# Kernel optimization log

Hardware: AMD Instinct MI355X
Metric: run time of the kernel (lower is better)

## Reference

```python
import jax, jax.numpy as jnp
import numpy as np

B, C, H, W = 16, 256, 96, 96
K = 3
K2 = K * K


def setup_inputs() -> dict:
    key = jax.random.key(0)
    ks = jax.random.split(key, 8)
    s = 1.0 / np.sqrt(C)  # fan-in style scale for 1x1 convs
    sk = 1.0 / np.sqrt(K2)
    return {
        "x": jax.random.normal(ks[0], (B, C, H, W), jnp.float32),
        "w_xproj": jax.random.normal(ks[1], (C, C), jnp.float32) * s,
        "b_xproj": jnp.zeros((C,), jnp.float32),
        "w_proj": jax.random.normal(ks[2], (C, C), jnp.float32) * s,
        "b_proj": jnp.zeros((C,), jnp.float32),
        "w_kp": jax.random.normal(ks[3], (C, C), jnp.float32) * s,
        "b_kp": jnp.zeros((C,), jnp.float32),
        "w_kg": jax.random.normal(ks[4], (K2, K2), jnp.float32) * sk,
        "b_kg": jnp.zeros((K2,), jnp.float32),
        "diff_ctrl": jnp.zeros((1, 1, 1, C), jnp.float32),
    }


def reference(x, w_xproj, b_xproj, w_proj, b_proj, w_kp, b_kp, w_kg, b_kg, diff_ctrl):
    b, c, h, w = x.shape
    # --- kernel synthesis ---
    # 1x1 conv (kernel_proj)
    kp = jnp.einsum('bchw,oc->bohw', x, w_kp) + b_kp[None, :, None, None]
    # AdaptiveAvgPool1d over flattened spatial dim -> 9 bins (H*W divisible by 9)
    pooled = kp.reshape(b, c, K2, (h * w) // K2).mean(axis=-1)  # [B, C, 9]
    pooled = jax.nn.gelu(pooled)
    # per-channel Linear(9 -> 9): y = W @ v + b
    ker = jnp.einsum('bck,jk->bcj', pooled, w_kg) + b_kg  # [B, C, 9]
    # rearrange 'c (k1 k2) -> k1 k2 1 c' (batched)
    ker = ker.reshape(b, c, K, K).transpose(0, 2, 3, 1)[:, :, :, None, :]  # [B, K, K, 1, C]
    # lateral inhibition: subtract learned fraction of per-channel kernel mean
    factor = jax.nn.sigmoid(diff_ctrl)  # [1, 1, 1, C]
    ker = ker - factor * ker.mean(axis=(1, 2, 3), keepdims=True)
    # --- main path ---
    xp = jnp.einsum('bchw,oc->bohw', x, w_xproj) + b_xproj[None, :, None, None]
    pad = K // 2

    def dwconv(xi, ki):  # xi [C,H,W], ki [K,K,1,C]
        return jax.lax.conv_general_dilated(
            xi[None], ki, window_strides=(1, 1),
            padding=((pad, pad), (pad, pad)),
            dimension_numbers=('NCHW', 'HWIO', 'NCHW'),
            feature_group_count=c)[0]

    y = jax.vmap(dwconv)(xp, ker)  # per-sample dynamic depthwise conv
    out = jnp.einsum('bchw,oc->bohw', y, w_proj) + b_proj[None, :, None, None]
    return out
```

## Files before the change

kernel.cpp:

```cpp
#include <hip/hip_runtime.h>

#define CCH 256
#define HWP 9216
#define IMGDIM 96

typedef __attribute__((ext_vector_type(8))) short s16x8;
typedef __attribute__((ext_vector_type(4))) float f32x4;

__device__ __forceinline__ unsigned short f2bf(float f){
  unsigned u = __float_as_uint(f);
  u += 0x7fffu + ((u >> 16) & 1u);
  return (unsigned short)(u >> 16);
}
__device__ __forceinline__ float bf2f(unsigned short h){
  return __uint_as_float(((unsigned)h) << 16);
}

__global__ void k0_convert(const float* __restrict__ wx, const float* __restrict__ wp,
                           unsigned short* __restrict__ wxb, unsigned short* __restrict__ wpb){
  int i = blockIdx.x * 256 + threadIdx.x;
  wxb[i] = f2bf(wx[i]);
  wpb[i] = f2bf(wp[i]);
}

__device__ __forceinline__ void gemm_core(const unsigned short* __restrict__ wbf,
                                          const unsigned short* lds_x,
                                          f32x4 acc[4][4], int lane, int obase){
  const int g = lane >> 4, r = lane & 15;
  #pragma unroll
  for (int k0 = 0; k0 < 256; k0 += 32){
    s16x8 afr[4], bfr[4];
    #pragma unroll
    for (int nf = 0; nf < 4; ++nf){
      int p = nf*16 + r;
      unsigned off = (unsigned)(p*512 + (k0 + g*8)*2) ^ ((unsigned)(p & 7) << 4);
      bfr[nf] = *(const s16x8*)((const char*)lds_x + off);
    }
    #pragma unroll
    for (int mf = 0; mf < 4; ++mf){
      afr[mf] = *(const s16x8*)(wbf + (size_t)(obase + mf*16 + r)*CCH + k0 + g*8);
    }
    #pragma unroll
    for (int mf = 0; mf < 4; ++mf){
      #pragma unroll
      for (int nf = 0; nf < 4; ++nf){
        acc[mf][nf] = __builtin_amdgcn_mfma_f32_16x16x32_bf16(afr[mf], bfr[nf], acc[mf][nf], 0, 0, 0);
      }
    }
  }
}

__global__ __launch_bounds__(256) void k1_xproj(const float* __restrict__ x,
    const unsigned short* __restrict__ wxb, const float* __restrict__ bx,
    unsigned short* __restrict__ xp, float* __restrict__ xpart){
  const int tile = blockIdx.x, b = blockIdx.y;
  const int p0 = tile * 64;
  const int t = threadIdx.x;
  const int lane = t & 63, wave = t >> 6;
  __shared__ __align__(16) unsigned short xlds[64*256];

  const float* xb = x + (size_t)b * CCH * HWP;
  const int binj = p0 >> 10;
  const int blk  = (p0 >> 6) & 15;
  const int pg = t & 15;
  const int cgl = t >> 4;

  #pragma unroll
  for (int i = 0; i < 4; ++i){
    const int c0 = (i*16 + cgl) * 4;
    const int pl = pg * 4;
    float v[4][4];
    #pragma unroll
    for (int ci = 0; ci < 4; ++ci){
      float4 q = *(const float4*)(xb + (size_t)(c0 + ci)*HWP + p0 + pl);
      v[ci][0]=q.x; v[ci][1]=q.y; v[ci][2]=q.z; v[ci][3]=q.w;
    }
    #pragma unroll
    for (int pj = 0; pj < 4; ++pj){
      const int p = pl + pj;
      unsigned off = (unsigned)(p*512 + c0*2) ^ ((unsigned)(p & 7) << 4);
      ushort4 pk;
      pk.x = f2bf(v[0][pj]); pk.y = f2bf(v[1][pj]);
      pk.z = f2bf(v[2][pj]); pk.w = f2bf(v[3][pj]);
      *(ushort4*)((char*)xlds + off) = pk;
    }
    #pragma unroll
    for (int ci = 0; ci < 4; ++ci){
      float s = v[ci][0] + v[ci][1] + v[ci][2] + v[ci][3];
      s += __shfl_xor(s, 1); s += __shfl_xor(s, 2);
      s += __shfl_xor(s, 4); s += __shfl_xor(s, 8);
      if ((lane & 15) == 0){
        xpart[(((size_t)b*9 + binj)*16 + blk)*CCH + (c0 + ci)] = s;
      }
    }
  }
  __syncthreads();

  f32x4 acc[4][4];
  f32x4 zz = {0.f,0.f,0.f,0.f};
  #pragma unroll
  for (int i2=0;i2<4;++i2){
    #pragma unroll
    for (int j2=0;j2<4;++j2) acc[i2][j2] = zz;
  }
  gemm_core(wxb, xlds, acc, lane, wave*64);

  const int g = lane >> 4, r = lane & 15;
  #pragma unroll
  for (int mf = 0; mf < 4; ++mf){
    const int o = wave*64 + mf*16 + 4*g;
    float b0 = bx[o], b1 = bx[o+1], b2 = bx[o+2], b3 = bx[o+3];
    #pragma unroll
    for (int nf = 0; nf < 4; ++nf){
      const int p = p0 + nf*16 + r;
      ushort4 pk;
      pk.x = f2bf(acc[mf][nf][0] + b0);
      pk.y = f2bf(acc[mf][nf][1] + b1);
      pk.z = f2bf(acc[mf][nf][2] + b2);
      pk.w = f2bf(acc[mf][nf][3] + b3);
      *(ushort4*)(xp + ((size_t)b*HWP + p)*CCH + o) = pk;
    }
  }
}

__global__ __launch_bounds__(256) void k2a_pooled(const float* __restrict__ xpart,
    const float* __restrict__ wkp, const float* __restrict__ bkp,
    float* __restrict__ pooledg){
  const int j = blockIdx.x, b = blockIdx.y, t = threadIdx.x;
  __shared__ float xbar[256];
  __shared__ float wch[256][65];
  const float* xp0 = xpart + (((size_t)b*9 + j)*16)*CCH;
  float s = 0.f;
  #pragma unroll
  for (int blk = 0; blk < 16; ++blk) s += xp0[blk*CCH + t];
  xbar[t] = s * (1.0f/1024.0f);
  float acc = bkp[t];
  for (int ch = 0; ch < 4; ++ch){
    __syncthreads();
    for (int u = t; u < 256*64; u += 256){
      wch[u >> 6][u & 63] = wkp[(size_t)(u >> 6)*CCH + ch*64 + (u & 63)];
    }
    __syncthreads();
    #pragma unroll
    for (int c = 0; c < 64; ++c) acc += wch[t][c] * xbar[ch*64 + c];
  }
  float x3 = acc*acc*acc;
  float tg = tanhf(0.7978845608028654f*(acc + 0.044715f*x3));
  pooledg[((size_t)b*9 + j)*CCH + t] = 0.5f*acc*(1.0f + tg);
}

__global__ void k2b_ker(const float* __restrict__ pooledg, const float* __restrict__ wkg,
                        const float* __restrict__ bkg, const float* __restrict__ dctrl,
                        float* __restrict__ kerg){
  const int b = blockIdx.x, c = threadIdx.x;
  float pl[9];
  #pragma unroll
  for (int k = 0; k < 9; ++k) pl[k] = pooledg[((size_t)b*9 + k)*CCH + c];
  float kv[9]; float m = 0.f;
  #pragma unroll
  for (int jp = 0; jp < 9; ++jp){
    float s2 = bkg[jp];
    #pragma unroll
    for (int k = 0; k < 9; ++k) s2 += pl[k] * wkg[jp*9 + k];
    kv[jp] = s2; m += s2;
  }
  m *= (1.0f/9.0f);
  float f = 1.0f / (1.0f + expf(-dctrl[c]));
  #pragma unroll
  for (int jp = 0; jp < 9; ++jp) kerg[((size_t)b*9 + jp)*CCH + c] = kv[jp] - f*m;
}

__global__ __launch_bounds__(256) void k3_conv(const unsigned short* __restrict__ xp,
    const unsigned short* __restrict__ wpb, const float* __restrict__ bp,
    const float* __restrict__ kerg, float* __restrict__ out){
  const int tile = blockIdx.x, b = blockIdx.y;
  const int th0 = (tile / 12) * 8, tw0 = (tile % 12) * 8;
  const int t = threadIdx.x, lane = t & 63, wave = t >> 6;
  __shared__ __align__(16) unsigned short halo[100*128];
  __shared__ __align__(16) unsigned short ylds[64*256];
  __shared__ __align__(16) float kl[9][256];

  for (int u = t; u < 9*256; u += 256)
    kl[u >> 8][u & 255] = kerg[((size_t)b*9 + (u >> 8))*CCH + (u & 255)];

  const unsigned short* xpb = xp + (size_t)b * HWP * CCH;
  const int p = t & 63, dh = p >> 3, dw = p & 7;
  const int clb = (t >> 6) * 32;

  for (int chunk = 0; chunk < 2; ++chunk){
    __syncthreads();
    for (int u = t; u < 1600; u += 256){
      const int pos = u >> 4, w16 = u & 15;
      const int rr = pos / 10, cc = pos % 10;
      const int hh = th0 + rr - 1, ww = tw0 + cc - 1;
      uint4 val = {0u,0u,0u,0u};
      if (hh >= 0 && hh < IMGDIM && ww >= 0 && ww < IMGDIM)
        val = *(const uint4*)(xpb + ((size_t)(hh*IMGDIM + ww))*CCH + chunk*128 + w16*8);
      unsigned off = (unsigned)(pos*256 + w16*16) ^ ((unsigned)(pos & 7) << 4);
      *(uint4*)((char*)halo + off) = val;
    }
    __syncthreads();
    #pragma unroll
    for (int ci = 0; ci < 4; ++ci){
      const int cl = clb + ci*8;
      const int cg = chunk*128 + cl;
      float a8[8] = {0,0,0,0,0,0,0,0};
      #pragma unroll
      for (int tap = 0; tap < 9; ++tap){
        const int pos = (dh + tap/3)*10 + (dw + tap%3);
        unsigned hof = (unsigned)(pos*256 + cl*2) ^ ((unsigned)(pos & 7) << 4);
        union { uint4 q; unsigned short u16[8]; } hv;
        hv.q = *(const uint4*)((const char*)halo + hof);
        const float4* kp4 = (const float4*)&kl[tap][cg];
        float4 ka = kp4[0], kb = kp4[1];
        a8[0] += bf2f(hv.u16[0]) * ka.x;
        a8[1] += bf2f(hv.u16[1]) * ka.y;
        a8[2] += bf2f(hv.u16[2]) * ka.z;
        a8[3] += bf2f(hv.u16[3]) * ka.w;
        a8[4] += bf2f(hv.u16[4]) * kb.x;
        a8[5] += bf2f(hv.u16[5]) * kb.y;
        a8[6] += bf2f(hv.u16[6]) * kb.z;
        a8[7] += bf2f(hv.u16[7]) * kb.w;
      }
      unsigned pk[4];
      #pragma unroll
      for (int e = 0; e < 4; ++e)
        pk[e] = (unsigned)f2bf(a8[2*e]) | ((unsigned)f2bf(a8[2*e+1]) << 16);
      unsigned yoff = (unsigned)(p*512 + cg*2) ^ ((unsigned)(p & 7) << 4);
      *(uint4*)((char*)ylds + yoff) = *(uint4*)pk;
    }
  }
  __syncthreads();

  f32x4 acc[4][4];
  f32x4 zz = {0.f,0.f,0.f,0.f};
  #pragma unroll
  for (int i2=0;i2<4;++i2){
    #pragma unroll
    for (int j2=0;j2<4;++j2) acc[i2][j2] = zz;
  }
  gemm_core(wpb, ylds, acc, lane, wave*64);

  const int g = lane >> 4, r = lane & 15;
  #pragma unroll
  for (int mf = 0; mf < 4; ++mf){
    const int o = wave*64 + mf*16 + 4*g;
    float b0 = bp[o], b1 = bp[o+1], b2 = bp[o+2], b3 = bp[o+3];
    #pragma unroll
    for (int nf = 0; nf < 4; ++nf){
      const int pl2 = nf*16 + r;
      const int hh = th0 + (pl2 >> 3), ww = tw0 + (pl2 & 7);
      const size_t pix = (size_t)hh*IMGDIM + ww;
      out[((size_t)b*CCH + o + 0)*HWP + pix] = acc[mf][nf][0] + b0;
      out[((size_t)b*CCH + o + 1)*HWP + pix] = acc[mf][nf][1] + b1;
      out[((size_t)b*CCH + o + 2)*HWP + pix] = acc[mf][nf][2] + b2;
      out[((size_t)b*CCH + o + 3)*HWP + pix] = acc[mf][nf][3] + b3;
    }
  }
}

extern "C" void kernel_launch(void* const* d_in, const int* in_sizes, int n_in,
                              void* d_out, int out_size, void* d_ws, size_t ws_size,
                              hipStream_t stream){
  const float* x   = (const float*)d_in[0];
  const float* wxp = (const float*)d_in[1];
  const float* bxp = (const float*)d_in[2];
  const float* wpr = (const float*)d_in[3];
  const float* bpr = (const float*)d_in[4];
  const float* wkp = (const float*)d_in[5];
  const float* bkp = (const float*)d_in[6];
  const float* wkg = (const float*)d_in[7];
  const float* bkg = (const float*)d_in[8];
  const float* dct = (const float*)d_in[9];

  char* ws = (char*)d_ws;
  unsigned short* xp    = (unsigned short*)(ws);
  float*          xpart = (float*)(ws + 75497472);
  float*          pooled= (float*)(ws + 77856768);
  float*          kerg  = (float*)(ws + 78004224);
  unsigned short* wxb   = (unsigned short*)(ws + 78151680);
  unsigned short* wpb   = (unsigned short*)(ws + 78282752);
  float* o = (float*)d_out;

  k0_convert<<<256, 256, 0, stream>>>(wxp, wpr, wxb, wpb);
  k1_xproj<<<dim3(144,16), 256, 0, stream>>>(x, wxb, bxp, xp, xpart);
  k2a_pooled<<<dim3(9,16), 256, 0, stream>>>(xpart, wkp, bkp, pooled);
  k2b_ker<<<16, 256, 0, stream>>>(pooled, wkg, bkg, dct, kerg);
  k3_conv<<<dim3(144,16), 256, 0, stream>>>(xp, wpb, bpr, kerg, o);
}
```

Measured before the change: 278.0 us.

## Split fused depthwise+projection kernel and stage xproj stores through LDS

The fused depthwise-conv plus 1x1 projection kernel is split into two kernels: a depthwise conv that writes a bf16 intermediate buffer, then a separate GEMM projection. The split only runs when the workspace is large enough, otherwise the fused kernel is kept. The xproj epilogue now stages its output tile through a swizzled LDS buffer so global stores are full 16-byte contiguous writes. The split trades an extra round trip through global memory (about 75MB of writes and reads) for simpler kernels with less LDS per block and possibly higher occupancy.

```diff
diff --git a/kernel.cpp b/kernel.cpp
--- a/kernel.cpp
+++ b/kernel.cpp
@@ -105,20 +105,36 @@
   }
   gemm_core(wxb, xlds, acc, lane, wave*64);
 
-  const int g = lane >> 4, r = lane & 15;
-  #pragma unroll
-  for (int mf = 0; mf < 4; ++mf){
-    const int o = wave*64 + mf*16 + 4*g;
-    float b0 = bx[o], b1 = bx[o+1], b2 = bx[o+2], b3 = bx[o+3];
-    #pragma unroll
-    for (int nf = 0; nf < 4; ++nf){
-      const int p = p0 + nf*16 + r;
-      ushort4 pk;
-      pk.x = f2bf(acc[mf][nf][0] + b0);
-      pk.y = f2bf(acc[mf][nf][1] + b1);
-      pk.z = f2bf(acc[mf][nf][2] + b2);
-      pk.w = f2bf(acc[mf][nf][3] + b3);
-      *(ushort4*)(xp + ((size_t)b*HWP + p)*CCH + o) = pk;
+  __syncthreads();
+  {
+    const int g = lane >> 4, r = lane & 15;
+    #pragma unroll
+    for (int mf = 0; mf < 4; ++mf){
+      const int o = wave*64 + mf*16 + 4*g;
+      float b0 = bx[o], b1 = bx[o+1], b2 = bx[o+2], b3 = bx[o+3];
+      #pragma unroll
+      for (int nf = 0; nf < 4; ++nf){
+        const int p = nf*16 + r;
+        unsigned off = (unsigned)(p*512 + o*2) ^ ((unsigned)(p & 7) << 4);
+        ushort4 pk;
+        pk.x = f2bf(acc[mf][nf][0] + b0);
+        pk.y = f2bf(acc[mf][nf][1] + b1);
+        pk.z = f2bf(acc[mf][nf][2] + b2);
+        pk.w = f2bf(acc[mf][nf][3] + b3);
+        *(ushort4*)((char*)xlds + off) = pk;
+      }
+    }
+  }
+  __syncthreads();
+  {
+    const size_t gbase = ((size_t)b*HWP + p0)*CCH;
+    #pragma unroll
+    for (int it = 0; it < 8; ++it){
+      const unsigned u = it*256 + t;
+      const unsigned p = u >> 5;
+      const unsigned srcoff = (u*16u) ^ ((p & 7) << 4);
+      uint4 v = *(const uint4*)((const char*)xlds + srcoff);
+      *(uint4*)(xp + gbase + (size_t)u*8) = v;
     }
   }
 }
@@ -168,6 +184,112 @@
   float f = 1.0f / (1.0f + expf(-dctrl[c]));
   #pragma unroll
   for (int jp = 0; jp < 9; ++jp) kerg[((size_t)b*9 + jp)*CCH + c] = kv[jp] - f*m;
+}
+
+__global__ __launch_bounds__(256) void k3a_dw(const unsigned short* __restrict__ xp,
+    const float* __restrict__ kerg, unsigned short* __restrict__ y){
+  const int tile = blockIdx.x, b = blockIdx.y;
+  const int th0 = (tile / 12) * 8, tw0 = (tile % 12) * 8;
+  const int t = threadIdx.x;
+  __shared__ __align__(16) unsigned short halo[100*128];
+  __shared__ float kl[9][256];
+
+  for (int u = t; u < 9*256; u += 256)
+    kl[u >> 8][u & 255] = kerg[((size_t)b*9 + (u >> 8))*CCH + (u & 255)];
+
+  const unsigned short* xpb = xp + (size_t)b * HWP * CCH;
+  unsigned short* yb = y + (size_t)b * HWP * CCH;
+  const int p = t >> 2;
+  const int dh = p >> 3, dw = p & 7;
+  const int cl = (t & 3) * 8;
+  const size_t pout = (size_t)((th0 + dh)*IMGDIM + (tw0 + dw))*CCH;
+
+  for (int chunk = 0; chunk < 2; ++chunk){
+    __syncthreads();
+    for (int u = t; u < 1600; u += 256){
+      const int pos = u >> 4, w16 = u & 15;
+      const int rr = pos / 10, cc = pos % 10;
+      const int hh = th0 + rr - 1, ww = tw0 + cc - 1;
+      uint4 val = {0u,0u,0u,0u};
+      if (hh >= 0 && hh < IMGDIM && ww >= 0 && ww < IMGDIM)
+        val = *(const uint4*)(xpb + ((size_t)(hh*IMGDIM + ww))*CCH + chunk*128 + w16*8);
+      unsigned off = (unsigned)(pos*256 + w16*16) ^ ((unsigned)(pos & 7) << 4);
+      *(uint4*)((char*)halo + off) = val;
+    }
+    __syncthreads();
+    #pragma unroll
+    for (int ci = 0; ci < 4; ++ci){
+      const int c = cl + ci*32;
+      const int cg = chunk*128 + c;
+      float a8[8] = {0,0,0,0,0,0,0,0};
+      #pragma unroll
+      for (int tap = 0; tap < 9; ++tap){
+        const int pos = (dh + tap/3)*10 + (dw + tap%3);
+        unsigned hof = (unsigned)(pos*256 + c*2) ^ ((unsigned)(pos & 7) << 4);
+        union { uint4 q; unsigned short u16[8]; } hv;
+        hv.q = *(const uint4*)((const char*)halo + hof);
+        const float4* kp4 = (const float4*)&kl[tap][cg];
+        float4 ka = kp4[0], kb = kp4[1];
+        a8[0] += bf2f(hv.u16[0]) * ka.x;
+        a8[1] += bf2f(hv.u16[1]) * ka.y;
+        a8[2] += bf2f(hv.u16[2]) * ka.z;
+        a8[3] += bf2f(hv.u16[3]) * ka.w;
+        a8[4] += bf2f(hv.u16[4]) * kb.x;
+        a8[5] += bf2f(hv.u16[5]) * kb.y;
+        a8[6] += bf2f(hv.u16[6]) * kb.z;
+        a8[7] += bf2f(hv.u16[7]) * kb.w;
+      }
+      unsigned pk[4];
+      #pragma unroll
+      for (int e = 0; e < 4; ++e)
+        pk[e] = (unsigned)f2bf(a8[2*e]) | ((unsigned)f2bf(a8[2*e+1]) << 16);
+      *(uint4*)(yb + pout + cg) = *(uint4*)pk;
+    }
+  }
+}
+
+__global__ __launch_bounds__(256) void k3b_proj(const unsigned short* __restrict__ y,
+    const unsigned short* __restrict__ wpb, const float* __restrict__ bp,
+    float* __restrict__ out){
+  const int tile = blockIdx.x, b = blockIdx.y;
+  const int p0 = tile * 64;
+  const int t = threadIdx.x, lane = t & 63, wave = t >> 6;
+  __shared__ __align__(16) unsigned short ylds[64*256];
+  const unsigned short* yb = y + (size_t)b * HWP * CCH;
+
+  #pragma unroll
+  for (int it = 0; it < 8; ++it){
+    const unsigned u = it*256 + t;
+    const unsigned p = u >> 5;
+    const unsigned c16 = (u & 31) ^ (p & 7);
+    uint4 v = *(const uint4*)(yb + (size_t)(p0 + p)*CCH + c16*8);
+    *(uint4*)((char*)ylds + (size_t)u*16) = v;
+  }
+  __syncthreads();
+
+  f32x4 acc[4][4];
+  f32x4 zz = {0.f,0.f,0.f,0.f};
+  #pragma unroll
+  for (int i2=0;i2<4;++i2){
+    #pragma unroll
+    for (int j2=0;j2<4;++j2) acc[i2][j2] = zz;
+  }
+  gemm_core(wpb, ylds, acc, lane, wave*64);
+
+  const int g = lane >> 4, r = lane & 15;
+  #pragma unroll
+  for (int mf = 0; mf < 4; ++mf){
+    const int o = wave*64 + mf*16 + 4*g;
+    float b0 = bp[o], b1 = bp[o+1], b2 = bp[o+2], b3 = bp[o+3];
+    #pragma unroll
+    for (int nf = 0; nf < 4; ++nf){
+      const int pp = p0 + nf*16 + r;
+      out[((size_t)b*CCH + o + 0)*HWP + pp] = acc[mf][nf][0] + b0;
+      out[((size_t)b*CCH + o + 1)*HWP + pp] = acc[mf][nf][1] + b1;
+      out[((size_t)b*CCH + o + 2)*HWP + pp] = acc[mf][nf][2] + b2;
+      out[((size_t)b*CCH + o + 3)*HWP + pp] = acc[mf][nf][3] + b3;
+    }
+  }
 }
 
 __global__ __launch_bounds__(256) void k3_conv(const unsigned short* __restrict__ xp,
@@ -274,17 +396,24 @@
   const float* dct = (const float*)d_in[9];
 
   char* ws = (char*)d_ws;
-  unsigned short* xp    = (unsigned short*)(ws);
-  float*          xpart = (float*)(ws + 75497472);
-  float*          pooled= (float*)(ws + 77856768);
-  float*          kerg  = (float*)(ws + 78004224);
-  unsigned short* wxb   = (unsigned short*)(ws + 78151680);
-  unsigned short* wpb   = (unsigned short*)(ws + 78282752);
+  unsigned short* wxb   = (unsigned short*)(ws + 0);
+  unsigned short* wpb   = (unsigned short*)(ws + 131072);
+  float*          xpart = (float*)(ws + 262144);
+  float*          pooled= (float*)(ws + 2621440);
+  float*          kerg  = (float*)(ws + 2768896);
+  unsigned short* xp    = (unsigned short*)(ws + 2916352);
+  unsigned short* ybuf  = (unsigned short*)(ws + 78413824);
+  const size_t need_split = 153911296;
   float* o = (float*)d_out;
 
   k0_convert<<<256, 256, 0, stream>>>(wxp, wpr, wxb, wpb);
   k1_xproj<<<dim3(144,16), 256, 0, stream>>>(x, wxb, bxp, xp, xpart);
   k2a_pooled<<<dim3(9,16), 256, 0, stream>>>(xpart, wkp, bkp, pooled);
   k2b_ker<<<16, 256, 0, stream>>>(pooled, wkg, bkg, dct, kerg);
-  k3_conv<<<dim3(144,16), 256, 0, stream>>>(xp, wpb, bpr, kerg, o);
-}
+  if (ws_size >= need_split){
+    k3a_dw<<<dim3(144,16), 256, 0, stream>>>(xp, kerg, ybuf);
+    k3b_proj<<<dim3(144,16), 256, 0, stream>>>(ybuf, wpb, bpr, o);
+  } else {
+    k3_conv<<<dim3(144,16), 256, 0, stream>>>(xp, wpb, bpr, kerg, o);
+  }
+}
```

Result: faster. 238.7 us (-14.1%).

## Split depthwise conv and projection, double-buffer LDS channel chunks, stage epilogue stores

Applied to the files above, without the earlier changes.

The xproj GEMM now streams channel chunks of 64 through double-buffered LDS, loading the next chunk while computing the current one. Its output goes out through an LDS staging buffer so global stores are coalesced. The fused conv+proj kernel is split into a depthwise kernel, which writes a bf16 intermediate to global memory, and a separate pipelined projection GEMM kernel with contiguous 64-pixel tiles. The goal is to cut LDS footprint and raise occupancy, and to overlap loads with compute. The cost is an extra intermediate round-trip through HBM, roughly 75MB written and read, plus an extra launch.

```diff
diff --git a/kernel.cpp b/kernel.cpp
--- a/kernel.cpp
+++ b/kernel.cpp
@@ -23,23 +23,23 @@
   wpb[i] = f2bf(wp[i]);
 }
 
-__device__ __forceinline__ void gemm_core(const unsigned short* __restrict__ wbf,
-                                          const unsigned short* lds_x,
-                                          f32x4 acc[4][4], int lane, int obase){
+__device__ __forceinline__ void gemm_chunk(const unsigned short* __restrict__ wbf,
+                                           const unsigned short* buf,
+                                           f32x4 acc[4][4], int lane, int obase, int c0){
   const int g = lane >> 4, r = lane & 15;
   #pragma unroll
-  for (int k0 = 0; k0 < 256; k0 += 32){
+  for (int kk = 0; kk < 2; ++kk){
+    const int kc = kk*32 + g*8;
     s16x8 afr[4], bfr[4];
     #pragma unroll
     for (int nf = 0; nf < 4; ++nf){
-      int p = nf*16 + r;
-      unsigned off = (unsigned)(p*512 + (k0 + g*8)*2) ^ ((unsigned)(p & 7) << 4);
-      bfr[nf] = *(const s16x8*)((const char*)lds_x + off);
-    }
-    #pragma unroll
-    for (int mf = 0; mf < 4; ++mf){
-      afr[mf] = *(const s16x8*)(wbf + (size_t)(obase + mf*16 + r)*CCH + k0 + g*8);
-    }
+      const int p = nf*16 + r;
+      unsigned off = (unsigned)(p*128 + kc*2) ^ ((unsigned)(p & 7) << 4);
+      bfr[nf] = *(const s16x8*)((const char*)buf + off);
+    }
+    #pragma unroll
+    for (int mf = 0; mf < 4; ++mf)
+      afr[mf] = *(const s16x8*)(wbf + (size_t)(obase + mf*16 + r)*CCH + c0 + kc);
     #pragma unroll
     for (int mf = 0; mf < 4; ++mf){
       #pragma unroll
@@ -50,52 +50,48 @@
   }
 }
 
+__device__ __forceinline__ void k1_load(const float* __restrict__ xb, int p0, int c0,
+                                        int pg, int cgl, float v[4][4]){
+  #pragma unroll
+  for (int ci = 0; ci < 4; ++ci){
+    float4 q = *(const float4*)(xb + (size_t)(c0 + cgl*4 + ci)*HWP + p0 + pg*4);
+    v[ci][0]=q.x; v[ci][1]=q.y; v[ci][2]=q.z; v[ci][3]=q.w;
+  }
+}
+__device__ __forceinline__ void k1_store(unsigned short* buf, int pg, int cgl, float v[4][4],
+                                         float* __restrict__ xpart, int c0, int lane, int bbase){
+  #pragma unroll
+  for (int pj = 0; pj < 4; ++pj){
+    const int p = pg*4 + pj;
+    unsigned off = (unsigned)(p*128 + cgl*8) ^ ((unsigned)(p & 7) << 4);
+    ushort4 pk;
+    pk.x = f2bf(v[0][pj]); pk.y = f2bf(v[1][pj]);
+    pk.z = f2bf(v[2][pj]); pk.w = f2bf(v[3][pj]);
+    *(ushort4*)((char*)buf + off) = pk;
+  }
+  #pragma unroll
+  for (int ci = 0; ci < 4; ++ci){
+    float s = v[ci][0] + v[ci][1] + v[ci][2] + v[ci][3];
+    s += __shfl_xor(s, 1); s += __shfl_xor(s, 2);
+    s += __shfl_xor(s, 4); s += __shfl_xor(s, 8);
+    if ((lane & 15) == 0) xpart[bbase + c0 + cgl*4 + ci] = s;
+  }
+}
+
 __global__ __launch_bounds__(256) void k1_xproj(const float* __restrict__ x,
     const unsigned short* __restrict__ wxb, const float* __restrict__ bx,
     unsigned short* __restrict__ xp, float* __restrict__ xpart){
   const int tile = blockIdx.x, b = blockIdx.y;
   const int p0 = tile * 64;
-  const int t = threadIdx.x;
-  const int lane = t & 63, wave = t >> 6;
-  __shared__ __align__(16) unsigned short xlds[64*256];
+  const int t = threadIdx.x, lane = t & 63, wave = t >> 6;
+  __shared__ __align__(16) unsigned short xlds[2][64*64];
 
   const float* xb = x + (size_t)b * CCH * HWP;
-  const int binj = p0 >> 10;
-  const int blk  = (p0 >> 6) & 15;
-  const int pg = t & 15;
-  const int cgl = t >> 4;
-
-  #pragma unroll
-  for (int i = 0; i < 4; ++i){
-    const int c0 = (i*16 + cgl) * 4;
-    const int pl = pg * 4;
-    float v[4][4];
-    #pragma unroll
-    for (int ci = 0; ci < 4; ++ci){
-      float4 q = *(const float4*)(xb + (size_t)(c0 + ci)*HWP + p0 + pl);
-      v[ci][0]=q.x; v[ci][1]=q.y; v[ci][2]=q.z; v[ci][3]=q.w;
-    }
-    #pragma unroll
-    for (int pj = 0; pj < 4; ++pj){
-      const int p = pl + pj;
-      unsigned off = (unsigned)(p*512 + c0*2) ^ ((unsigned)(p & 7) << 4);
-      ushort4 pk;
-      pk.x = f2bf(v[0][pj]); pk.y = f2bf(v[1][pj]);
-      pk.z = f2bf(v[2][pj]); pk.w = f2bf(v[3][pj]);
-      *(ushort4*)((char*)xlds + off) = pk;
-    }
-    #pragma unroll
-    for (int ci = 0; ci < 4; ++ci){
-      float s = v[ci][0] + v[ci][1] + v[ci][2] + v[ci][3];
-      s += __shfl_xor(s, 1); s += __shfl_xor(s, 2);
-      s += __shfl_xor(s, 4); s += __shfl_xor(s, 8);
-      if ((lane & 15) == 0){
-        xpart[(((size_t)b*9 + binj)*16 + blk)*CCH + (c0 + ci)] = s;
-      }
-    }
-  }
-  __syncthreads();
-
+  const int binj = p0 >> 10, blk = (p0 >> 6) & 15;
+  const int bbase = (((int)b*9 + binj)*16 + blk)*CCH;
+  const int pg = t & 15, cgl = t >> 4;
+
+  float v[2][4][4];
   f32x4 acc[4][4];
   f32x4 zz = {0.f,0.f,0.f,0.f};
   #pragma unroll
@@ -103,22 +99,52 @@
     #pragma unroll
     for (int j2=0;j2<4;++j2) acc[i2][j2] = zz;
   }
-  gemm_core(wxb, xlds, acc, lane, wave*64);
-
+
+  k1_load(xb, p0, 0, pg, cgl, v[0]);
+  k1_store(xlds[0], pg, cgl, v[0], xpart, 0, lane, bbase);
+
+  #pragma unroll
+  for (int ch = 0; ch < 4; ++ch){
+    __syncthreads();
+    if (ch < 3) k1_load(xb, p0, (ch+1)*64, pg, cgl, v[(ch+1)&1]);
+    gemm_chunk(wxb, xlds[ch & 1], acc, lane, wave*64, ch*64);
+    if (ch < 3) k1_store(xlds[(ch+1)&1], pg, cgl, v[(ch+1)&1], xpart, (ch+1)*64, lane, bbase);
+  }
+
+  unsigned short* eb = &xlds[0][0];
   const int g = lane >> 4, r = lane & 15;
   #pragma unroll
-  for (int mf = 0; mf < 4; ++mf){
-    const int o = wave*64 + mf*16 + 4*g;
-    float b0 = bx[o], b1 = bx[o+1], b2 = bx[o+2], b3 = bx[o+3];
-    #pragma unroll
-    for (int nf = 0; nf < 4; ++nf){
-      const int p = p0 + nf*16 + r;
-      ushort4 pk;
-      pk.x = f2bf(acc[mf][nf][0] + b0);
-      pk.y = f2bf(acc[mf][nf][1] + b1);
-      pk.z = f2bf(acc[mf][nf][2] + b2);
-      pk.w = f2bf(acc[mf][nf][3] + b3);
-      *(ushort4*)(xp + ((size_t)b*HWP + p)*CCH + o) = pk;
+  for (int h = 0; h < 2; ++h){
+    __syncthreads();
+    if ((wave >> 1) == h){
+      const int mw = wave & 1;
+      #pragma unroll
+      for (int mf = 0; mf < 4; ++mf){
+        const int o  = mw*64 + mf*16 + 4*g;
+        const int og = h*128 + o;
+        float b0 = bx[og], b1 = bx[og+1], b2 = bx[og+2], b3 = bx[og+3];
+        #pragma unroll
+        for (int nf = 0; nf < 4; ++nf){
+          const int p = nf*16 + r;
+          unsigned off = (unsigned)(p*256 + o*2) ^ ((unsigned)(p & 7) << 4);
+          ushort4 pk;
+          pk.x = f2bf(acc[mf][nf][0] + b0);
+          pk.y = f2bf(acc[mf][nf][1] + b1);
+          pk.z = f2bf(acc[mf][nf][2] + b2);
+          pk.w = f2bf(acc[mf][nf][3] + b3);
+          *(ushort4*)((char*)eb + off) = pk;
+        }
+      }
+    }
+    __syncthreads();
+    const size_t gb = ((size_t)b*HWP + p0)*CCH + h*128;
+    #pragma unroll
+    for (int it = 0; it < 4; ++it){
+      const unsigned u = it*256 + t;
+      const unsigned p = u >> 4, unit = u & 15;
+      const unsigned srcoff = (u*16u) ^ ((p & 7) << 4);
+      uint4 val = *(const uint4*)((const char*)eb + srcoff);
+      *(uint4*)(xp + gb + (size_t)p*CCH + unit*8) = val;
     }
   }
 }
@@ -170,47 +196,67 @@
   for (int jp = 0; jp < 9; ++jp) kerg[((size_t)b*9 + jp)*CCH + c] = kv[jp] - f*m;
 }
 
-__global__ __launch_bounds__(256) void k3_conv(const unsigned short* __restrict__ xp,
-    const unsigned short* __restrict__ wpb, const float* __restrict__ bp,
-    const float* __restrict__ kerg, float* __restrict__ out){
+__global__ __launch_bounds__(256) void k3a_dw(const unsigned short* __restrict__ xp,
+    const float* __restrict__ kerg, unsigned short* __restrict__ y){
   const int tile = blockIdx.x, b = blockIdx.y;
   const int th0 = (tile / 12) * 8, tw0 = (tile % 12) * 8;
-  const int t = threadIdx.x, lane = t & 63, wave = t >> 6;
-  __shared__ __align__(16) unsigned short halo[100*128];
-  __shared__ __align__(16) unsigned short ylds[64*256];
-  __shared__ __align__(16) float kl[9][256];
+  const int t = threadIdx.x;
+  __shared__ __align__(16) unsigned short halo[2][100*64];
+  __shared__ float kl[9][256];
 
   for (int u = t; u < 9*256; u += 256)
     kl[u >> 8][u & 255] = kerg[((size_t)b*9 + (u >> 8))*CCH + (u & 255)];
 
   const unsigned short* xpb = xp + (size_t)b * HWP * CCH;
-  const int p = t & 63, dh = p >> 3, dw = p & 7;
-  const int clb = (t >> 6) * 32;
-
-  for (int chunk = 0; chunk < 2; ++chunk){
-    __syncthreads();
-    for (int u = t; u < 1600; u += 256){
-      const int pos = u >> 4, w16 = u & 15;
-      const int rr = pos / 10, cc = pos % 10;
-      const int hh = th0 + rr - 1, ww = tw0 + cc - 1;
-      uint4 val = {0u,0u,0u,0u};
-      if (hh >= 0 && hh < IMGDIM && ww >= 0 && ww < IMGDIM)
-        val = *(const uint4*)(xpb + ((size_t)(hh*IMGDIM + ww))*CCH + chunk*128 + w16*8);
-      unsigned off = (unsigned)(pos*256 + w16*16) ^ ((unsigned)(pos & 7) << 4);
-      *(uint4*)((char*)halo + off) = val;
-    }
-    __syncthreads();
-    #pragma unroll
-    for (int ci = 0; ci < 4; ++ci){
-      const int cl = clb + ci*8;
-      const int cg = chunk*128 + cl;
+  unsigned short* yb = y + (size_t)b * HWP * CCH;
+  const int p = t >> 2, dh = p >> 3, dw = p & 7, q = t & 3;
+  const size_t pout = (size_t)((th0 + dh)*IMGDIM + (tw0 + dw))*CCH;
+
+  uint4 sreg[4];
+
+  #define K3A_ISSUE(CH)                                                        \
+    _Pragma("unroll")                                                          \
+    for (int i = 0; i < 4; ++i){                                               \
+      const int u = i*256 + t;                                                 \
+      if (u < 800){                                                            \
+        const int pos = u >> 3, w8 = u & 7;                                    \
+        const int rr = pos / 10, cc = pos % 10;                                \
+        const int hh = th0 + rr - 1, ww = tw0 + cc - 1;                        \
+        uint4 val = {0u,0u,0u,0u};                                             \
+        if (hh >= 0 && hh < IMGDIM && ww >= 0 && ww < IMGDIM)                  \
+          val = *(const uint4*)(xpb + ((size_t)(hh*IMGDIM + ww))*CCH + (CH)*64 + w8*8); \
+        sreg[i] = val;                                                         \
+      }                                                                        \
+    }
+  #define K3A_WRITE(BUF)                                                       \
+    _Pragma("unroll")                                                          \
+    for (int i = 0; i < 4; ++i){                                               \
+      const int u = i*256 + t;                                                 \
+      if (u < 800){                                                            \
+        const int pos = u >> 3, w8 = u & 7;                                    \
+        unsigned off = (unsigned)(pos*128 + w8*16) ^ ((unsigned)(pos & 7) << 4); \
+        *(uint4*)((char*)halo[BUF] + off) = sreg[i];                           \
+      }                                                                        \
+    }
+
+  K3A_ISSUE(0)
+  K3A_WRITE(0)
+
+  #pragma unroll
+  for (int ch = 0; ch < 4; ++ch){
+    __syncthreads();
+    if (ch < 3) K3A_ISSUE(ch+1)
+    #pragma unroll
+    for (int ci = 0; ci < 2; ++ci){
+      const int c = q*16 + ci*8;
+      const int cg = ch*64 + c;
       float a8[8] = {0,0,0,0,0,0,0,0};
       #pragma unroll
       for (int tap = 0; tap < 9; ++tap){
         const int pos = (dh + tap/3)*10 + (dw + tap%3);
-        unsigned hof = (unsigned)(pos*256 + cl*2) ^ ((unsigned)(pos & 7) << 4);
-        union { uint4 q; unsigned short u16[8]; } hv;
-        hv.q = *(const uint4*)((const char*)halo + hof);
+        unsigned hof = (unsigned)(pos*128 + c*2) ^ ((unsigned)(pos & 7) << 4);
+        union { uint4 qv; unsigned short u16[8]; } hv;
+        hv.qv = *(const uint4*)((const char*)halo[ch & 1] + hof);
         const float4* kp4 = (const float4*)&kl[tap][cg];
         float4 ka = kp4[0], kb = kp4[1];
         a8[0] += bf2f(hv.u16[0]) * ka.x;
@@ -226,11 +272,37 @@
       #pragma unroll
       for (int e = 0; e < 4; ++e)
         pk[e] = (unsigned)f2bf(a8[2*e]) | ((unsigned)f2bf(a8[2*e+1]) << 16);
-      unsigned yoff = (unsigned)(p*512 + cg*2) ^ ((unsigned)(p & 7) << 4);
-      *(uint4*)((char*)ylds + yoff) = *(uint4*)pk;
-    }
-  }
-  __syncthreads();
+      *(uint4*)(yb + pout + cg) = *(uint4*)pk;
+    }
+    if (ch < 3) K3A_WRITE((ch+1)&1)
+  }
+  #undef K3A_ISSUE
+  #undef K3A_WRITE
+}
+
+__global__ __launch_bounds__(256) void k3b_proj(const unsigned short* __restrict__ y,
+    const unsigned short* __restrict__ wpb, const float* __restrict__ bp,
+    float* __restrict__ out){
+  const int tile = blockIdx.x, b = blockIdx.y;
+  const int p0 = tile * 64;
+  const int t = threadIdx.x, lane = t & 63, wave = t >> 6;
+  __shared__ __align__(16) unsigned short ylds[2][64*64];
+  const unsigned short* yb = y + (size_t)b * HWP * CCH;
+
+  const int ug = t & 7, pg2 = t >> 3;
+  uint4 srg[2];
+
+  #define K3B_ISSUE(CH)                                                        \
+    _Pragma("unroll")                                                          \
+    for (int i = 0; i < 2; ++i)                                                \
+      srg[i] = *(const uint4*)(yb + (size_t)(p0 + pg2 + i*32)*CCH + (CH)*64 + ug*8);
+  #define K3B_WRITE(BUF)                                                       \
+    _Pragma("unroll")                                                          \
+    for (int i = 0; i < 2; ++i){                                               \
+      const int p = pg2 + i*32;                                                \
+      unsigned off = (unsigned)(p*128 + ug*16) ^ ((unsigned)(p & 7) << 4);     \
+      *(uint4*)((char*)ylds[BUF] + off) = srg[i];                              \
+    }
 
   f32x4 acc[4][4];
   f32x4 zz = {0.f,0.f,0.f,0.f};
@@ -239,7 +311,19 @@
     #pragma unroll
     for (int j2=0;j2<4;++j2) acc[i2][j2] = zz;
   }
-  gemm_core(wpb, ylds, acc, lane, wave*64);
+
+  K3B_ISSUE(0)
+  K3B_WRITE(0)
+
+  #pragma unroll
+  for (int ch = 0; ch < 4; ++ch){
+    __syncthreads();
+    if (ch < 3) K3B_ISSUE(ch+1)
+    gemm_chunk(wpb, ylds[ch & 1], acc, lane, wave*64, ch*64);
+    if (ch < 3) K3B_WRITE((ch+1)&1)
+  }
+  #undef K3B_ISSUE
+  #undef K3B_WRITE
 
   const int g = lane >> 4, r = lane & 15;
   #pragma unroll
@@ -248,13 +332,11 @@
     float b0 = bp[o], b1 = bp[o+1], b2 = bp[o+2], b3 = bp[o+3];
     #pragma unroll
     for (int nf = 0; nf < 4; ++nf){
-      const int pl2 = nf*16 + r;
-      const int hh = th0 + (pl2 >> 3), ww = tw0 + (pl2 & 7);
-      const size_t pix = (size_t)hh*IMGDIM + ww;
-      out[((size_t)b*CCH + o + 0)*HWP + pix] = acc[mf][nf][0] + b0;
-      out[((size_t)b*CCH + o + 1)*HWP + pix] = acc[mf][nf][1] + b1;
-      out[((size_t)b*CCH + o + 2)*HWP + pix] = acc[mf][nf][2] + b2;
-      out[((size_t)b*CCH + o + 3)*HWP + pix] = acc[mf][nf][3] + b3;
+      const int pp = p0 + nf*16 + r;
+      out[((size_t)b*CCH + o + 0)*HWP + pp] = acc[mf][nf][0] + b0;
+      out[((size_t)b*CCH + o + 1)*HWP + pp] = acc[mf][nf][1] + b1;
+      out[((size_t)b*CCH + o + 2)*HWP + pp] = acc[mf][nf][2] + b2;
+      out[((size_t)b*CCH + o + 3)*HWP + pp] = acc[mf][nf][3] + b3;
     }
   }
 }
@@ -274,17 +356,19 @@
   const float* dct = (const float*)d_in[9];
 
   char* ws = (char*)d_ws;
-  unsigned short* xp    = (unsigned short*)(ws);
-  float*          xpart = (float*)(ws + 75497472);
-  float*          pooled= (float*)(ws + 77856768);
-  float*          kerg  = (float*)(ws + 78004224);
-  unsigned short* wxb   = (unsigned short*)(ws + 78151680);
-  unsigned short* wpb   = (unsigned short*)(ws + 78282752);
+  unsigned short* wxb   = (unsigned short*)(ws + 0);
+  unsigned short* wpb   = (unsigned short*)(ws + 131072);
+  float*          xpart = (float*)(ws + 262144);
+  float*          pooled= (float*)(ws + 2621440);
+  float*          kerg  = (float*)(ws + 2768896);
+  unsigned short* xp    = (unsigned short*)(ws + 2916352);
+  unsigned short* ybuf  = (unsigned short*)(ws + 78413824);
   float* o = (float*)d_out;
 
   k0_convert<<<256, 256, 0, stream>>>(wxp, wpr, wxb, wpb);
   k1_xproj<<<dim3(144,16), 256, 0, stream>>>(x, wxb, bxp, xp, xpart);
   k2a_pooled<<<dim3(9,16), 256, 0, stream>>>(xpart, wkp, bkp, pooled);
   k2b_ker<<<16, 256, 0, stream>>>(pooled, wkg, bkg, dct, kerg);
-  k3_conv<<<dim3(144,16), 256, 0, stream>>>(xp, wpb, bpr, kerg, o);
-}
+  k3a_dw<<<dim3(144,16), 256, 0, stream>>>(xp, kerg, ybuf);
+  k3b_proj<<<dim3(144,16), 256, 0, stream>>>(ybuf, wpb, bpr, o);
+}
```

After: 235.7 us. 15.2% less time.
